# Kernel tuning notes

Hardware: AMD Instinct MI355X
Metric: run time of the kernel (lower is better)

Reference implementation:

```python
import jax, jax.numpy as jnp
import numpy as np

NUM_USERS = 200000
NUM_PRODUCTS = 100000
N_NODES = NUM_USERS + NUM_PRODUCTS
N_EDGES = 1000000
USER_FDIM = 128
PROD_FDIM = 128
EDIM = 64


def setup_inputs() -> dict:
    key = jax.random.key(0)
    ks = jax.random.split(key, 16)
    s = 0.02
    inp = {
        "edge_index": jnp.stack([
            jax.random.randint(ks[0], (N_EDGES,), 0, NUM_USERS, dtype=jnp.int32).astype(jnp.int64),
            jax.random.randint(ks[1], (N_EDGES,), 0, NUM_PRODUCTS, dtype=jnp.int32).astype(jnp.int64),
        ], axis=0),
        "user_features": jax.random.normal(ks[2], (NUM_USERS, USER_FDIM), jnp.float32),
        "product_features": jax.random.normal(ks[3], (NUM_PRODUCTS, PROD_FDIM), jnp.float32),
        "user_emb": jax.random.normal(ks[4], (NUM_USERS, EDIM), jnp.float32) * s,
        "product_emb": jax.random.normal(ks[5], (NUM_PRODUCTS, EDIM), jnp.float32) * s,
        "W_uf": jax.random.normal(ks[6], (USER_FDIM, EDIM), jnp.float32) * s,
        "b_uf": jnp.zeros((EDIM,), jnp.float32),
        "W_pf": jax.random.normal(ks[7], (PROD_FDIM, EDIM), jnp.float32) * s,
        "b_pf": jnp.zeros((EDIM,), jnp.float32),
        "conv1_W": jax.random.normal(ks[8], (EDIM, EDIM), jnp.float32) * s,
        "conv1_b": jnp.zeros((EDIM,), jnp.float32),
        "conv2_W": jax.random.normal(ks[9], (EDIM, EDIM), jnp.float32) * s,
        "conv2_b": jnp.zeros((EDIM,), jnp.float32),
        "pred_W1": jax.random.normal(ks[10], (2 * EDIM, EDIM), jnp.float32) * s,
        "pred_b1": jnp.zeros((EDIM,), jnp.float32),
        "pred_W2": jax.random.normal(ks[11], (EDIM, 1), jnp.float32) * s,
        "pred_b2": jnp.zeros((1,), jnp.float32),
    }
    return inp


def _gcn_conv(x, W, b, row, col, n_nodes):
    # PyG GCNConv: h = x W; out[col] += deg^-1/2[row] * deg^-1/2[col] * h[row]; + b
    h = x @ W
    deg = jax.ops.segment_sum(jnp.ones_like(col, dtype=x.dtype), col, num_segments=n_nodes)
    dis = jnp.where(deg > 0, jax.lax.rsqrt(jnp.maximum(deg, 1.0)), 0.0)
    norm = dis[row] * dis[col]                     # [E_total]
    msgs = h[row] * norm[:, None]                  # gather + edge weight
    out = jax.ops.segment_sum(msgs, col, num_segments=n_nodes)  # scatter-add
    return out + b


def reference(edge_index, user_features, product_features, user_emb, product_emb,
              W_uf, b_uf, W_pf, b_pf, conv1_W, conv1_b, conv2_W, conv2_b,
              pred_W1, pred_b1, pred_W2, pred_b2):
    user_idx = edge_index[0]
    prod_idx = edge_index[1]

    user_x = user_features @ W_uf + b_uf + user_emb          # [Nu, D]
    prod_x = product_features @ W_pf + b_pf + product_emb    # [Np, D]
    x = jnp.concatenate([user_x, prod_x], axis=0)            # [N, D]

    # symmetrized edges + self-loops (GCNConv default add_self_loops=True)
    ar = jnp.arange(N_NODES, dtype=edge_index.dtype)
    row = jnp.concatenate([user_idx, prod_idx, ar])
    col = jnp.concatenate([prod_idx, user_idx, ar])

    x = jax.nn.relu(_gcn_conv(x, conv1_W, conv1_b, row, col, N_NODES))
    # dropout p=0.2 is identity in eval mode
    x = _gcn_conv(x, conv2_W, conv2_b, row, col, N_NODES)

    user_e = x[:NUM_USERS][user_idx]                          # [E, D]
    prod_e = x[NUM_USERS:][prod_idx]                          # [E, D]
    pair = jnp.concatenate([user_e, prod_e], axis=1)          # [E, 2D]
    h = jax.nn.relu(pair @ pred_W1 + pred_b1)
    logits = h @ pred_W2 + pred_b2                            # [E, 1]
    preds = jax.nn.sigmoid(logits).squeeze(-1) * 5.0
    return preds
```

## Files before the change

kernel.cpp:

```cpp
#include <hip/hip_runtime.h>
#include <math.h>

#define NUM_USERS 200000
#define NUM_PRODUCTS 100000
#define N_NODES 300000
#define N_EDGES 1000000
#define EDIM 64
#define FDIM 128
#define CAP 40
#define FILL_T 250000
#define LDST 72
#define NT_U 12500
#define NT_ALL 18750
#define ZERO_BLK 1172

typedef __attribute__((ext_vector_type(8))) short short8;
typedef __attribute__((ext_vector_type(4))) float f32x4;

static __device__ inline short f2bf(float f) {
    unsigned int u = __float_as_uint(f);
    unsigned int r = (u + 0x7FFFu + ((u >> 16) & 1u)) >> 16;
    return (short)r;
}
static __device__ inline float bf2f(unsigned short s) {
    return __uint_as_float(((unsigned int)s) << 16);
}
static __device__ inline float disf(int c) {
    return rsqrtf(1.0f + (float)c);
}

__global__ void k_setup(int* __restrict__ cnt,
                        const float* __restrict__ W_uf, const float* __restrict__ W_pf,
                        const float* __restrict__ c1, const float* __restrict__ c2,
                        const float* __restrict__ W1, short* __restrict__ wts) {
    int b = blockIdx.x;
    if (b < ZERO_BLK) {
        int i = b * 256 + threadIdx.x;
        if (i < 300032) cnt[i] = 0;
        return;
    }
    int gid = (b - ZERO_BLK) * 256 + threadIdx.x;
    if (gid >= 32768) return;
    if (gid < 8192) {
        int n = gid >> 7, k = gid & 127;
        wts[gid] = f2bf(W_uf[k * 64 + n]);
    } else if (gid < 16384) {
        int i = gid - 8192; int n = i >> 7, k = i & 127;
        wts[gid] = f2bf(W_pf[k * 64 + n]);
    } else if (gid < 20480) {
        int i = gid - 16384; int n = i >> 6, k = i & 63;
        wts[gid] = f2bf(c1[k * 64 + n]);
    } else if (gid < 24576) {
        int i = gid - 20480; int n = i >> 6, k = i & 63;
        wts[gid] = f2bf(c2[k * 64 + n]);
    } else {
        int i = gid - 24576; int n = i >> 7, k = i & 127;
        wts[gid] = f2bf(W1[k * 64 + n]);
    }
}

__global__ __launch_bounds__(256) void k_fill_direct(
    const int* __restrict__ ei, int* __restrict__ cnt, int* __restrict__ adj) {
    int t = blockIdx.x * 256 + threadIdx.x;
    if (t >= FILL_T) return;
    int u[4], p[4], pu[4], pp[4];
#pragma unroll
    for (int j = 0; j < 4; ++j) {
        int e = t + j * FILL_T;
        u[j] = ei[e];
        p[j] = ei[N_EDGES + e];
    }
#pragma unroll
    for (int j = 0; j < 4; ++j) {
        pp[j] = atomicAdd(&cnt[p[j]], 1);
        pu[j] = atomicAdd(&cnt[u[j]], 1);
    }
#pragma unroll
    for (int j = 0; j < 4; ++j) {
        adj[(size_t)p[j] * CAP + pp[j]] = u[j];
        adj[(size_t)u[j] * CAP + pu[j]] = p[j];
    }
}

__global__ __launch_bounds__(256) void k_xform_c1(
    const float* __restrict__ user_feat, const float* __restrict__ prod_feat,
    const short* __restrict__ wts,
    const float* __restrict__ b_uf, const float* __restrict__ b_pf,
    const float* __restrict__ user_emb, const float* __restrict__ prod_emb,
    const int* __restrict__ cnt, unsigned short* __restrict__ h) {
    __shared__ unsigned short lds[4][16 * LDST];
    int tid = threadIdx.x;
    int wave = tid >> 6;
    int tile = blockIdx.x * 4 + wave;
    if (tile >= NT_ALL) tile = NT_ALL - 1;
    int lane = tid & 63, ln = lane & 15, quad = lane >> 4;

    const float* feat; const short* WT; const float* b; const float* emb;
    int node_off, mtile;
    if (tile < NT_U) {
        feat = user_feat; WT = wts;        b = b_uf; emb = user_emb; node_off = 0;         mtile = tile;
    } else {
        feat = prod_feat; WT = wts + 8192; b = b_pf; emb = prod_emb; node_off = NUM_USERS; mtile = tile - NT_U;
    }
    const short* c1T = wts + 16384;

    short8 Bx[4][4];
#pragma unroll
    for (int t = 0; t < 4; ++t)
#pragma unroll
        for (int kk = 0; kk < 4; ++kk)
            Bx[t][kk] = *(const short8*)(WT + ((t * 16 + ln) * 128 + kk * 32 + quad * 8));
    short8 Bc[4][2];
#pragma unroll
    for (int t = 0; t < 4; ++t)
#pragma unroll
        for (int kk = 0; kk < 2; ++kk)
            Bc[t][kk] = *(const short8*)(c1T + ((t * 16 + ln) * 64 + kk * 32 + quad * 8));
    float bv[4];
#pragma unroll
    for (int t = 0; t < 4; ++t) bv[t] = b[t * 16 + ln];

    int mbase = mtile * 16;
    const float* arow = feat + (size_t)(mbase + ln) * FDIM + quad * 8;

    f32x4 acc[4] = {{0.f,0.f,0.f,0.f},{0.f,0.f,0.f,0.f},{0.f,0.f,0.f,0.f},{0.f,0.f,0.f,0.f}};
#pragma unroll
    for (int kk = 0; kk < 4; ++kk) {
        float4 lo = *(const float4*)(arow + kk * 32);
        float4 hi = *(const float4*)(arow + kk * 32 + 4);
        short8 Af;
        Af[0] = f2bf(lo.x); Af[1] = f2bf(lo.y); Af[2] = f2bf(lo.z); Af[3] = f2bf(lo.w);
        Af[4] = f2bf(hi.x); Af[5] = f2bf(hi.y); Af[6] = f2bf(hi.z); Af[7] = f2bf(hi.w);
#pragma unroll
        for (int t = 0; t < 4; ++t)
            acc[t] = __builtin_amdgcn_mfma_f32_16x16x32_bf16(Af, Bx[t][kk], acc[t], 0, 0, 0);
    }
#pragma unroll
    for (int r = 0; r < 4; ++r) {
        int node = mbase + quad * 4 + r;
#pragma unroll
        for (int t = 0; t < 4; ++t) {
            float v = acc[t][r] + bv[t] + emb[(size_t)node * EDIM + t * 16 + ln];
            lds[wave][(quad * 4 + r) * LDST + t * 16 + ln] = (unsigned short)f2bf(v);
        }
    }
    __syncthreads();
    f32x4 acch[4] = {{0.f,0.f,0.f,0.f},{0.f,0.f,0.f,0.f},{0.f,0.f,0.f,0.f},{0.f,0.f,0.f,0.f}};
#pragma unroll
    for (int kk = 0; kk < 2; ++kk) {
        short8 Af = *(const short8*)(&lds[wave][ln * LDST + kk * 32 + quad * 8]);
#pragma unroll
        for (int t = 0; t < 4; ++t)
            acch[t] = __builtin_amdgcn_mfma_f32_16x16x32_bf16(Af, Bc[t][kk], acch[t], 0, 0, 0);
    }
    float disv[4];
#pragma unroll
    for (int r = 0; r < 4; ++r) disv[r] = disf(cnt[node_off + mbase + quad * 4 + r]);
#pragma unroll
    for (int r = 0; r < 4; ++r) {
        int node = mbase + quad * 4 + r;
#pragma unroll
        for (int t = 0; t < 4; ++t)
            h[(size_t)(node_off + node) * EDIM + t * 16 + ln] =
                (unsigned short)f2bf(disv[r] * acch[t][r]);
    }
}

__global__ __launch_bounds__(256) void k_gather_c2(
    const int* __restrict__ adj, const int* __restrict__ cnt,
    const unsigned short* __restrict__ h,
    const float* __restrict__ b1, const short* __restrict__ c2T,
    unsigned short* __restrict__ hout) {
    __shared__ unsigned short lds[4][16 * LDST];
    int tid = threadIdx.x;
    int wave = tid >> 6;
    int tile = blockIdx.x * 4 + wave;
    if (tile >= N_NODES / 16) tile = N_NODES / 16 - 1;
    int lane = tid & 63, ln = lane & 15, quad = lane >> 4;
    const unsigned int* hp = (const unsigned int*)h;

    short8 Bc[4][2];
#pragma unroll
    for (int t = 0; t < 4; ++t)
#pragma unroll
        for (int kk = 0; kk < 2; ++kk)
            Bc[t][kk] = *(const short8*)(c2T + ((t * 16 + ln) * 64 + kk * 32 + quad * 8));

    int mbase = tile * 16;
    float2 bb0 = ((const float2*)b1)[ln];
    float2 bb1 = ((const float2*)b1)[16 + ln];

#pragma unroll 1
    for (int it = 0; it < 4; ++it) {
        int d = mbase + it * 4 + quad;
        const unsigned int* hrow = hp + (size_t)d * 32;
        unsigned int s0 = hrow[ln], s1 = hrow[16 + ln];
        float a0 = bf2f((unsigned short)s0);
        float a1 = bf2f((unsigned short)(s0 >> 16));
        float a2 = bf2f((unsigned short)s1);
        float a3 = bf2f((unsigned short)(s1 >> 16));
        int cd = cnt[d];
        const int* ap = adj + (size_t)d * CAP;
        int i = 0;
        for (; i + 1 < cd; i += 2) {
            int r0 = ap[i], r1 = ap[i + 1];
            unsigned int p00 = hp[(size_t)r0 * 32 + ln];
            unsigned int p01 = hp[(size_t)r0 * 32 + 16 + ln];
            unsigned int p10 = hp[(size_t)r1 * 32 + ln];
            unsigned int p11 = hp[(size_t)r1 * 32 + 16 + ln];
            a0 += bf2f((unsigned short)p00) + bf2f((unsigned short)p10);
            a1 += bf2f((unsigned short)(p00 >> 16)) + bf2f((unsigned short)(p10 >> 16));
            a2 += bf2f((unsigned short)p01) + bf2f((unsigned short)p11);
            a3 += bf2f((unsigned short)(p01 >> 16)) + bf2f((unsigned short)(p11 >> 16));
        }
        if (i < cd) {
            int r0 = ap[i];
            unsigned int p00 = hp[(size_t)r0 * 32 + ln];
            unsigned int p01 = hp[(size_t)r0 * 32 + 16 + ln];
            a0 += bf2f((unsigned short)p00);
            a1 += bf2f((unsigned short)(p00 >> 16));
            a2 += bf2f((unsigned short)p01);
            a3 += bf2f((unsigned short)(p01 >> 16));
        }
        float dv = disf(cd);
        float v0 = fmaxf(fmaf(dv, a0, bb0.x), 0.f);
        float v1 = fmaxf(fmaf(dv, a1, bb0.y), 0.f);
        float v2 = fmaxf(fmaf(dv, a2, bb1.x), 0.f);
        float v3 = fmaxf(fmaf(dv, a3, bb1.y), 0.f);
        unsigned int* lrow = (unsigned int*)&lds[wave][(it * 4 + quad) * LDST];
        lrow[ln] = ((unsigned int)(unsigned short)f2bf(v1) << 16)
                 | (unsigned int)(unsigned short)f2bf(v0);
        lrow[16 + ln] = ((unsigned int)(unsigned short)f2bf(v3) << 16)
                      | (unsigned int)(unsigned short)f2bf(v2);
    }
    __syncthreads();
    f32x4 acc[4] = {{0.f,0.f,0.f,0.f},{0.f,0.f,0.f,0.f},{0.f,0.f,0.f,0.f},{0.f,0.f,0.f,0.f}};
#pragma unroll
    for (int kk = 0; kk < 2; ++kk) {
        short8 Af = *(const short8*)(&lds[wave][ln * LDST + kk * 32 + quad * 8]);
#pragma unroll
        for (int t = 0; t < 4; ++t)
            acc[t] = __builtin_amdgcn_mfma_f32_16x16x32_bf16(Af, Bc[t][kk], acc[t], 0, 0, 0);
    }
    float disv[4];
#pragma unroll
    for (int r = 0; r < 4; ++r) disv[r] = disf(cnt[mbase + quad * 4 + r]);
#pragma unroll
    for (int r = 0; r < 4; ++r) {
        int node = mbase + quad * 4 + r;
#pragma unroll
        for (int t = 0; t < 4; ++t)
            hout[(size_t)node * EDIM + t * 16 + ln] = (unsigned short)f2bf(disv[r] * acc[t][r]);
    }
}

__global__ __launch_bounds__(256) void k_gather(
    const int* __restrict__ adj, const int* __restrict__ cnt,
    const unsigned short* __restrict__ h,
    const float* __restrict__ b, unsigned short* __restrict__ xout, int relu) {
    int d = blockIdx.x * 4 + (threadIdx.x >> 6);
    if (d >= N_NODES) return;
    int l = threadIdx.x & 63;
    int half = l >> 5, c2 = l & 31;
    const unsigned int* hp = (const unsigned int*)h;

    float ax = 0.f, ay = 0.f;
    if (half == 0) {
        unsigned int pr = hp[(size_t)d * 32 + c2];
        ax = bf2f((unsigned short)pr);
        ay = bf2f((unsigned short)(pr >> 16));
    }
    int c = cnt[d];
    const int* ap = adj + (size_t)d * CAP;
    int i = 0;
    for (; i + 3 < c; i += 4) {
        int s0 = ap[i + half];
        int s1 = ap[i + 2 + half];
        unsigned int p0 = hp[(size_t)s0 * 32 + c2];
        unsigned int p1 = hp[(size_t)s1 * 32 + c2];
        ax += bf2f((unsigned short)p0) + bf2f((unsigned short)p1);
        ay += bf2f((unsigned short)(p0 >> 16)) + bf2f((unsigned short)(p1 >> 16));
    }
    if (i + half < c) {
        unsigned int p0 = hp[(size_t)ap[i + half] * 32 + c2];
        ax += bf2f((unsigned short)p0);
        ay += bf2f((unsigned short)(p0 >> 16));
    }
    if (i + 2 + half < c) {
        unsigned int p0 = hp[(size_t)ap[i + 2 + half] * 32 + c2];
        ax += bf2f((unsigned short)p0);
        ay += bf2f((unsigned short)(p0 >> 16));
    }
    ax += __shfl_xor(ax, 32, 64);
    ay += __shfl_xor(ay, 32, 64);
    float dv = disf(c);
    float2 bb = ((const float2*)b)[c2];
    float v0 = fmaf(dv, ax, bb.x);
    float v1 = fmaf(dv, ay, bb.y);
    if (relu) { v0 = fmaxf(v0, 0.f); v1 = fmaxf(v1, 0.f); }
    if (half == 0) {
        unsigned int pk = ((unsigned int)(unsigned short)f2bf(v1) << 16)
                        | (unsigned int)(unsigned short)f2bf(v0);
        ((unsigned int*)xout)[(size_t)d * 32 + c2] = pk;
    }
}

__global__ __launch_bounds__(256) void k_pred_mfma(
    const int* __restrict__ ei, const unsigned short* __restrict__ x,
    const short* __restrict__ W1T, const float* __restrict__ b1,
    const float* __restrict__ W2, const float* __restrict__ b2,
    float* __restrict__ preds) {
    int tid = threadIdx.x;
    int wave = tid >> 6, lane = tid & 63;
    int ln = lane & 15, quad = lane >> 4;

    short8 Bf[4][4];
#pragma unroll
    for (int t = 0; t < 4; ++t)
#pragma unroll
        for (int kk = 0; kk < 4; ++kk)
            Bf[t][kk] = *(const short8*)(W1T + ((t * 16 + ln) * 128 + kk * 32 + quad * 8));

    float b1v[4], W2v[4];
#pragma unroll
    for (int t = 0; t < 4; ++t) {
        b1v[t] = b1[t * 16 + ln];
        W2v[t] = W2[t * 16 + ln];
    }
    float b2s = b2[0];

    const int n_tiles = N_EDGES / 16;
    int gw = blockIdx.x * 4 + wave;
    int nwaves = gridDim.x * 4;

    int cu = 0, cp = 0;
    if (gw < n_tiles) {
        cu = ei[gw * 16 + ln];
        cp = ei[N_EDGES + gw * 16 + ln] + NUM_USERS;
    }
    for (int tile = gw; tile < n_tiles; tile += nwaves) {
        int u = cu, p = cp;
        int nt = tile + nwaves;
        if (nt < n_tiles) {
            cu = ei[nt * 16 + ln];
            cp = ei[N_EDGES + nt * 16 + ln] + NUM_USERS;
        }
        short8 Af[4];
        Af[0] = *(const short8*)(x + (size_t)u * EDIM + quad * 8);
        Af[1] = *(const short8*)(x + (size_t)u * EDIM + 32 + quad * 8);
        Af[2] = *(const short8*)(x + (size_t)p * EDIM + quad * 8);
        Af[3] = *(const short8*)(x + (size_t)p * EDIM + 32 + quad * 8);

        f32x4 acc[4] = {{0.f,0.f,0.f,0.f},{0.f,0.f,0.f,0.f},{0.f,0.f,0.f,0.f},{0.f,0.f,0.f,0.f}};
#pragma unroll
        for (int kk = 0; kk < 4; ++kk)
#pragma unroll
            for (int t = 0; t < 4; ++t)
                acc[t] = __builtin_amdgcn_mfma_f32_16x16x32_bf16(Af[kk], Bf[t][kk], acc[t], 0, 0, 0);

        float out[4];
#pragma unroll
        for (int r = 0; r < 4; ++r) {
            float part = 0.f;
#pragma unroll
            for (int t = 0; t < 4; ++t) {
                float hv = fmaxf(acc[t][r] + b1v[t], 0.f);
                part = fmaf(hv, W2v[t], part);
            }
            part += __shfl_xor(part, 1, 64);
            part += __shfl_xor(part, 2, 64);
            part += __shfl_xor(part, 4, 64);
            part += __shfl_xor(part, 8, 64);
            out[r] = part;
        }
        if (ln == 0) {
            int ebase = tile * 16;
#pragma unroll
            for (int r = 0; r < 4; ++r) {
                float logit = out[r] + b2s;
                preds[ebase + quad * 4 + r] = 5.f / (1.f + expf(-logit));
            }
        }
    }
}

extern "C" void kernel_launch(void* const* d_in, const int* in_sizes, int n_in,
                              void* d_out, int out_size, void* d_ws, size_t ws_size,
                              hipStream_t stream) {
    const int*   ei        = (const int*)d_in[0];
    const float* user_feat = (const float*)d_in[1];
    const float* prod_feat = (const float*)d_in[2];
    const float* user_emb  = (const float*)d_in[3];
    const float* prod_emb  = (const float*)d_in[4];
    const float* W_uf      = (const float*)d_in[5];
    const float* b_uf      = (const float*)d_in[6];
    const float* W_pf      = (const float*)d_in[7];
    const float* b_pf      = (const float*)d_in[8];
    const float* conv1_W   = (const float*)d_in[9];
    const float* conv1_b   = (const float*)d_in[10];
    const float* conv2_W   = (const float*)d_in[11];
    const float* conv2_b   = (const float*)d_in[12];
    const float* pred_W1   = (const float*)d_in[13];
    const float* pred_b1   = (const float*)d_in[14];
    const float* pred_W2   = (const float*)d_in[15];
    const float* pred_b2   = (const float*)d_in[16];

    int* ws_i = (int*)d_ws;
    int*   cnt  = ws_i;
    int*   adj  = ws_i + 600064;
    unsigned short* xbuf = (unsigned short*)(ws_i + 12601344);
    unsigned short* hbuf = (unsigned short*)(ws_i + 22201344);
    short* wts = (short*)(ws_i + 31801344);
    float* preds = (float*)d_out;

    k_setup<<<ZERO_BLK + 128, 256, 0, stream>>>(cnt, W_uf, W_pf, conv1_W, conv2_W, pred_W1, wts);
    k_fill_direct<<<(FILL_T + 255) / 256, 256, 0, stream>>>(ei, cnt, adj);

    k_xform_c1<<<(NT_ALL + 3) / 4, 256, 0, stream>>>(user_feat, prod_feat, wts,
                                                     b_uf, b_pf, user_emb, prod_emb,
                                                     cnt, hbuf);

    k_gather_c2<<<(18750 + 3) / 4, 256, 0, stream>>>(adj, cnt, hbuf, conv1_b,
                                                     wts + 20480, xbuf);
    k_gather<<<N_NODES / 4, 256, 0, stream>>>(adj, cnt, xbuf, conv2_b, hbuf, 0);

    k_pred_mfma<<<2048, 256, 0, stream>>>(ei, hbuf, wts + 24576, pred_b1, pred_W2, pred_b2, preds);
}
```

Before: 724.0 us.

## Bucket edges by destination range before building adjacency lists

Replaces the direct atomic adjacency fill with two passes. The first pass bins the symmetrized edges into 80 destination-range buckets using shared-memory counters. The second pass builds the adjacency lists per bucket, with blocks mapped so each bucket is handled on one XCD, which keeps the atomics and adj writes local in cache. This adds an extra write and read of the binned edges through a scratch region aliased with xbuf, and edges past a bucket's fixed capacity would be silently dropped.

```diff
diff --git a/kernel.cpp b/kernel.cpp
--- a/kernel.cpp
+++ b/kernel.cpp
@@ -8,11 +8,14 @@
 #define EDIM 64
 #define FDIM 128
 #define CAP 40
-#define FILL_T 250000
 #define LDST 72
 #define NT_U 12500
 #define NT_ALL 18750
-#define ZERO_BLK 1172
+#define ZERO_BLK 1173
+#define NBUK 80
+#define BNODES 2500
+#define BINCAP 49152
+#define CSR_REP 4
 
 typedef __attribute__((ext_vector_type(8))) short short8;
 typedef __attribute__((ext_vector_type(4))) float f32x4;
@@ -36,7 +39,7 @@
     int b = blockIdx.x;
     if (b < ZERO_BLK) {
         int i = b * 256 + threadIdx.x;
-        if (i < 300032) cnt[i] = 0;
+        if (i < 300032 + NBUK) cnt[i] = 0;
         return;
     }
     int gid = (b - ZERO_BLK) * 256 + threadIdx.x;
@@ -59,26 +62,71 @@
     }
 }
 
-__global__ __launch_bounds__(256) void k_fill_direct(
-    const int* __restrict__ ei, int* __restrict__ cnt, int* __restrict__ adj) {
-    int t = blockIdx.x * 256 + threadIdx.x;
-    if (t >= FILL_T) return;
-    int u[4], p[4], pu[4], pp[4];
-#pragma unroll
-    for (int j = 0; j < 4; ++j) {
-        int e = t + j * FILL_T;
-        u[j] = ei[e];
-        p[j] = ei[N_EDGES + e];
-    }
-#pragma unroll
-    for (int j = 0; j < 4; ++j) {
-        pp[j] = atomicAdd(&cnt[p[j]], 1);
-        pu[j] = atomicAdd(&cnt[u[j]], 1);
-    }
-#pragma unroll
-    for (int j = 0; j < 4; ++j) {
-        adj[(size_t)p[j] * CAP + pp[j]] = u[j];
-        adj[(size_t)u[j] * CAP + pu[j]] = p[j];
+__global__ __launch_bounds__(256) void k_bin(
+    const int* __restrict__ ei, int* __restrict__ gcnt, int* __restrict__ gbin) {
+    __shared__ int lcnt[NBUK];
+    __shared__ int lbase[NBUK];
+    int tid = threadIdx.x;
+    if (tid < NBUK) lcnt[tid] = 0;
+    __syncthreads();
+    int e0 = (blockIdx.x * 256 + tid) * 4;
+    bool act = e0 < N_EDGES;
+    int d[8], s[8], rk[8], bk[8];
+    if (act) {
+        int4 uu = *(const int4*)(ei + e0);
+        int4 pp = *(const int4*)(ei + N_EDGES + e0);
+        d[0] = pp.x; s[0] = uu.x;  d[1] = uu.x; s[1] = pp.x;
+        d[2] = pp.y; s[2] = uu.y;  d[3] = uu.y; s[3] = pp.y;
+        d[4] = pp.z; s[4] = uu.z;  d[5] = uu.z; s[5] = pp.z;
+        d[6] = pp.w; s[6] = uu.w;  d[7] = uu.w; s[7] = pp.w;
+#pragma unroll
+        for (int j = 0; j < 8; ++j) {
+            bk[j] = d[j] / BNODES;
+            rk[j] = atomicAdd(&lcnt[bk[j]], 1);
+        }
+    }
+    __syncthreads();
+    if (tid < NBUK) lbase[tid] = atomicAdd(&gcnt[tid], lcnt[tid]);
+    __syncthreads();
+    if (act) {
+#pragma unroll
+        for (int j = 0; j < 8; ++j) {
+            int pos = lbase[bk[j]] + rk[j];
+            if (pos < BINCAP)
+                *(int2*)(gbin + ((size_t)bk[j] * BINCAP + pos) * 2) = make_int2(d[j], s[j]);
+        }
+    }
+}
+
+__global__ __launch_bounds__(256) void k_csr(
+    const int* __restrict__ gcnt, const int* __restrict__ gbin,
+    int* __restrict__ cnt, int* __restrict__ adj) {
+    int i = blockIdx.x;
+    int xcd = i & 7, k = i >> 3;
+    int bucket = (k % (NBUK / 8)) * 8 + xcd;
+    int rep = k / (NBUK / 8);
+    int n = gcnt[bucket];
+    const int* bb = gbin + (size_t)bucket * BINCAP * 2;
+    const int stride = CSR_REP * 256;
+    int idx = rep * 256 + threadIdx.x;
+    for (; idx + 3 * stride < n; idx += 4 * stride) {
+        int2 e0 = *(const int2*)(bb + (size_t)(idx)*2);
+        int2 e1 = *(const int2*)(bb + (size_t)(idx + stride) * 2);
+        int2 e2 = *(const int2*)(bb + (size_t)(idx + 2 * stride) * 2);
+        int2 e3 = *(const int2*)(bb + (size_t)(idx + 3 * stride) * 2);
+        int s0 = atomicAdd(&cnt[e0.x], 1);
+        int s1 = atomicAdd(&cnt[e1.x], 1);
+        int s2 = atomicAdd(&cnt[e2.x], 1);
+        int s3 = atomicAdd(&cnt[e3.x], 1);
+        adj[(size_t)e0.x * CAP + s0] = e0.y;
+        adj[(size_t)e1.x * CAP + s1] = e1.y;
+        adj[(size_t)e2.x * CAP + s2] = e2.y;
+        adj[(size_t)e3.x * CAP + s3] = e3.y;
+    }
+    for (; idx < n; idx += stride) {
+        int2 e = *(const int2*)(bb + (size_t)idx * 2);
+        int s = atomicAdd(&cnt[e.x], 1);
+        adj[(size_t)e.x * CAP + s] = e.y;
     }
 }
 
@@ -407,14 +455,17 @@
 
     int* ws_i = (int*)d_ws;
     int*   cnt  = ws_i;
+    int*   gcnt = ws_i + 300032;
     int*   adj  = ws_i + 600064;
     unsigned short* xbuf = (unsigned short*)(ws_i + 12601344);
+    int*   gbin = ws_i + 12601344;
     unsigned short* hbuf = (unsigned short*)(ws_i + 22201344);
     short* wts = (short*)(ws_i + 31801344);
     float* preds = (float*)d_out;
 
     k_setup<<<ZERO_BLK + 128, 256, 0, stream>>>(cnt, W_uf, W_pf, conv1_W, conv2_W, pred_W1, wts);
-    k_fill_direct<<<(FILL_T + 255) / 256, 256, 0, stream>>>(ei, cnt, adj);
+    k_bin<<<(N_EDGES / 4 + 255) / 256, 256, 0, stream>>>(ei, gcnt, gbin);
+    k_csr<<<NBUK * CSR_REP, 256, 0, stream>>>(gcnt, gbin, cnt, adj);
 
     k_xform_c1<<<(NT_ALL + 3) / 4, 256, 0, stream>>>(user_feat, prod_feat, wts,
                                                      b_uf, b_pf, user_emb, prod_emb,
```

After: 681.6 us. 1.06x faster.
